# Kernel optimization log

Measured on AMD Instinct MI355X. Metric: run time of the kernel, lower is better.

## Reference

```python
import jax, jax.numpy as jnp
import numpy as np

B, T, D_IN, D_SAE, K = 256, 8, 768, 8192, 32


def setup_inputs() -> dict:
    key = jax.random.key(0)
    k1, k2, k3 = jax.random.split(key, 3)
    x = jax.random.normal(k1, (B, T, D_IN), dtype=jnp.float32)
    # kaiming_uniform: bound = sqrt(6 / fan_in), fan_in = prod of trailing dims
    bound_e = float(np.sqrt(6.0 / (D_SAE * D_IN)))
    W_enc = jax.random.uniform(k2, (T, D_SAE, D_IN), jnp.float32, -bound_e, bound_e)
    bound_d = float(np.sqrt(6.0 / (D_IN * D_SAE)))
    W_dec = jax.random.uniform(k3, (T, D_IN, D_SAE), jnp.float32, -bound_d, bound_d)
    # decoder column normalization (norm over d_in axis), as in _normalize_decoder
    norms = jnp.clip(jnp.linalg.norm(W_dec, axis=1, keepdims=True), 1e-8)
    W_dec = W_dec / norms
    b_enc = jnp.zeros((T, D_SAE), jnp.float32)
    b_dec = jnp.zeros((T, D_IN), jnp.float32)
    return {"x": x, "W_enc": W_enc, "b_enc": b_enc, "W_dec": W_dec,
            "b_dec": b_dec, "k": K}


def reference(x, W_enc, b_enc, W_dec, b_dec, k):
    # x: (B, T, d_in)
    x_c = x - b_dec[None]                                   # (B, T, d)
    pre = jnp.einsum('btd,thd->bth', x_c, W_enc) + b_enc[None]  # (B, T, h)
    bt = pre.shape[0] * pre.shape[1]
    pre_flat = pre.reshape(bt, -1)
    topk_vals, topk_idx = jax.lax.top_k(pre_flat, k)        # (BT, k)
    rows = jnp.arange(bt)[:, None]
    u_flat = jnp.zeros_like(pre_flat).at[rows, topk_idx].set(jax.nn.relu(topk_vals))
    u = u_flat.reshape(pre.shape)                            # (B, T, h)
    x_hat = jnp.einsum('bth,tdh->btd', u, W_dec) + b_dec[None]
    recon_loss = jnp.mean(jnp.sum((x_hat - x) ** 2, axis=-1))
    return recon_loss, x_hat, u
```

## Files before the change

### kernel.cpp

```cpp
#include <hip/hip_runtime.h>
#include <cstdint>
#include <cstddef>

constexpr int B_SZ  = 256;
constexpr int T_SZ  = 8;
constexpr int DIN   = 768;
constexpr int DSAE  = 8192;
constexpr int KSEL  = 32;
constexpr int NROWS = B_SZ * T_SZ;
constexpr int CAND_CAP = 64;
constexpr int RCAP  = 32;
constexpr float EPS_W = 2e-4f;

constexpr size_t XC_SZ    = (size_t)NROWS * DIN;
constexpr size_t OFF_XC   = 0;
constexpr size_t OFF_XCB  = OFF_XC + XC_SZ;
constexpr size_t XCB_WORDS = XC_SZ / 2;
constexpr size_t OFF_SIDX = OFF_XCB + XCB_WORDS;
constexpr size_t OFF_SVAL = OFF_SIDX + (size_t)NROWS * KSEL;
constexpr size_t OFF_WT   = OFF_SVAL + (size_t)NROWS * KSEL;
constexpr size_t WT_WORDS = (size_t)T_SZ * DSAE * DIN / 2;
constexpr size_t WS_FAST_WORDS = OFF_WT + WT_WORDS;

typedef short bf16x8 __attribute__((ext_vector_type(8)));
typedef float f32x4  __attribute__((ext_vector_type(4)));

__device__ inline unsigned rne1(float x) {
  unsigned u = __float_as_uint(x);
  return (u + 0x7FFFu + ((u >> 16) & 1u)) >> 16;
}
__device__ inline float bf16tof(unsigned short v) {
  return __uint_as_float((unsigned)v << 16);
}

__global__ void k_zero(float* p) { *p = 0.f; }

__global__ __launch_bounds__(256) void k_xc(const float* __restrict__ x,
                                            const float* __restrict__ bdec,
                                            float* __restrict__ xc,
                                            unsigned short* __restrict__ xcb) {
  int n = NROWS * DIN;
  for (int i = blockIdx.x * 256 + threadIdx.x; i < n; i += gridDim.x * 256) {
    int d = i % DIN;
    int t = (i / DIN) & (T_SZ - 1);
    float v = x[i] - bdec[t * DIN + d];
    xc[i] = v;
    xcb[i] = (unsigned short)rne1(v);
  }
}

__global__ __launch_bounds__(256, 4) void k_encoder(const unsigned short* __restrict__ xcb,
                                                    const float* __restrict__ Wenc,
                                                    const float* __restrict__ benc,
                                                    float* __restrict__ pre) {
  const int t  = blockIdx.y;
  const int n0 = blockIdx.x * 64;
  constexpr int NS = DIN / 32;
  __shared__ __align__(16) short Bs[2][64 * 32];
  const int tid = threadIdx.x;

  const int srow = tid >> 2;
  const int sq   = tid & 3;
  const float* bG = Wenc + ((size_t)t * DSAE + n0 + srow) * DIN + sq * 8;
  const int sssw = (srow & 3) ^ ((srow >> 2) & 3);
  const int wOff = srow * 32 + ((sq ^ sssw) << 3);
  float4 r0, r1;
  auto loadB = [&](int s) {
    const float* p = bG + s * 32;
    r0 = *(const float4*)p; r1 = *(const float4*)(p + 4);
  };
  auto stage = [&](int buf) {
    uint4 U;
    U.x = rne1(r0.x) | (rne1(r0.y) << 16); U.y = rne1(r0.z) | (rne1(r0.w) << 16);
    U.z = rne1(r1.x) | (rne1(r1.y) << 16); U.w = rne1(r1.z) | (rne1(r1.w) << 16);
    *(uint4*)&Bs[buf][wOff] = U;
  };

  const int wm = tid >> 6, lane = tid & 63;
  const int l15 = lane & 15, kc = lane >> 4;
  const unsigned short* aBase =
      xcb + ((size_t)(wm * 64 + l15) * T_SZ + t) * DIN + kc * 8;
  constexpr size_t A_MI = (size_t)16 * T_SZ * DIN;
  int bOff[4];
#pragma unroll
  for (int ni = 0; ni < 4; ++ni) {
    int row = ni * 16 + l15;
    bOff[ni] = row * 32 + ((kc ^ ((row & 3) ^ ((row >> 2) & 3))) << 3);
  }

  f32x4 acc[4][4] = {};
  bf16x8 a[4];
  loadB(0); stage(0); loadB(1);
#pragma unroll
  for (int mi = 0; mi < 4; ++mi)
    a[mi] = *(const bf16x8*)(aBase + mi * A_MI);
  int cur = 0;
  for (int s = 0; s < NS; ++s) {
    __syncthreads();
    bf16x8 bf[4];
#pragma unroll
    for (int ni = 0; ni < 4; ++ni) bf[ni] = *(const bf16x8*)&Bs[cur][bOff[ni]];
#pragma unroll
    for (int mi = 0; mi < 4; ++mi)
#pragma unroll
      for (int ni = 0; ni < 4; ++ni)
        acc[mi][ni] = __builtin_amdgcn_mfma_f32_16x16x32_bf16(
            a[mi], bf[ni], acc[mi][ni], 0, 0, 0);
    if (s + 1 < NS) {
      stage(cur ^ 1);
#pragma unroll
      for (int mi = 0; mi < 4; ++mi)
        a[mi] = *(const bf16x8*)(aBase + (s + 1) * 32 + mi * A_MI);
      if (s + 2 < NS) loadB(s + 2);
    }
    cur ^= 1;
  }

#pragma unroll
  for (int ni = 0; ni < 4; ++ni) {
    const int col = n0 + ni * 16 + l15;
    const float bias = benc[(size_t)t * DSAE + col];
#pragma unroll
    for (int mi = 0; mi < 4; ++mi) {
      const int rbase = wm * 64 + mi * 16 + kc * 4;
#pragma unroll
      for (int j = 0; j < 4; ++j)
        pre[((size_t)(rbase + j) * T_SZ + t) * DSAE + col] = acc[mi][ni][j] + bias;
    }
  }
}

__global__ __launch_bounds__(256) void k_select(const float* __restrict__ xc,
                                                const float* __restrict__ Wenc,
                                                const float* __restrict__ benc,
                                                float* u,
                                                int* __restrict__ sel_idx,
                                                float* __restrict__ sel_val) {
  const int r = blockIdx.x, t = r & (T_SZ - 1);
  __shared__ float sp[DSAE];
  __shared__ float redf[4], redf2[4];
  __shared__ int   redi[4];
  __shared__ float cv[CAND_CAP]; __shared__ int ci[CAND_CAP];
  __shared__ float sv[CAND_CAP]; __shared__ int si[CAND_CAP];
  __shared__ float rv[RCAP];     __shared__ int ri[RCAP];
  __shared__ double rd[RCAP];
  __shared__ double xd[DIN];
  __shared__ int   s_n, s_nR, s_A, s_nW;
  const int tid = threadIdx.x, lane = tid & 63, w = tid >> 6;
  float* urow = u + (size_t)r * DSAE;

  float s1 = 0.f, s2 = 0.f;
  for (int sgm = 0; sgm < DSAE / 256; ++sgm) {
    float v = urow[tid + sgm * 256];
    sp[tid + sgm * 256] = v;
    s1 += v; s2 = fmaf(v, v, s2);
  }
  for (int off = 32; off; off >>= 1) {
    s1 += __shfl_down(s1, off); s2 += __shfl_down(s2, off);
  }
  if (lane == 0) { redf[w] = s1; redf2[w] = s2; }
  __syncthreads();
  const float mean = (redf[0] + redf[1] + redf[2] + redf[3]) * (1.f / DSAE);
  const float var  = (redf2[0] + redf2[1] + redf2[2] + redf2[3]) * (1.f / DSAE) - mean * mean;
  const float sd   = sqrtf(fmaxf(var, 1e-20f));

  auto countGE = [&](float th) -> int {
    int c = 0;
#pragma unroll
    for (int sgm = 0; sgm < DSAE / 256; ++sgm)
      c += (sp[tid + sgm * 256] >= th) ? 1 : 0;
    for (int off = 32; off; off >>= 1) c += __shfl_down(c, off);
    __syncthreads();
    if (lane == 0) redi[w] = c;
    __syncthreads();
    return redi[0] + redi[1] + redi[2] + redi[3];
  };

  float tlo = mean + 2.0f * sd, thi = mean + 3.5f * sd;
  for (int it = 0; it < 8 && countGE(tlo) < KSEL; ++it) tlo -= sd;
  float th = mean + 2.52f * sd;
  int c = countGE(th);
  for (int it = 0; it < 24 && (c < KSEL || c > CAND_CAP); ++it) {
    if (c > CAND_CAP) tlo = th; else thi = th;
    th = 0.5f * (tlo + thi);
    c = countGE(th);
  }
  if (c < KSEL) { th = tlo; c = countGE(th); }

  if (tid == 0) s_n = 0;
  __syncthreads();
  for (int sgm = 0; sgm < DSAE / 256; ++sgm) {
    int i = tid + sgm * 256;
    float v = sp[i];
    if (v >= th) {
      int p = atomicAdd(&s_n, 1);
      if (p < CAND_CAP) { cv[p] = v; ci[p] = i; }
    }
  }
  __syncthreads();
  const int n = s_n < CAND_CAP ? s_n : CAND_CAP;

  if (tid < n) {
    float v = cv[tid]; int id = ci[tid];
    int rk = 0;
    for (int j = 0; j < n; ++j) {
      float vj = cv[j];
      rk += (vj > v || (vj == v && ci[j] < id)) ? 1 : 0;
    }
    sv[rk] = v; si[rk] = id;
  }
  __syncthreads();

  const float v32 = sv[KSEL - 1];
  const float wlo = v32 - EPS_W, whi = v32 + EPS_W;
  if (tid == 0) {
    int A = 0;
    while (A < KSEL - 1 && sv[A] > whi) ++A;
    s_A = A;
    int e = A;
    while (e < n && sv[e] >= wlo) ++e;
    s_nW = e - A;
  }
  __syncthreads();
  const int A  = s_A;
  const int nW = s_nW < RCAP ? s_nW : RCAP;
  if (tid < nW) { rv[tid] = sv[A + tid]; ri[tid] = si[A + tid]; }
  if (tid == 0) s_nR = nW;
  __syncthreads();
  if (th > wlo) {
    for (int sgm = 0; sgm < DSAE / 256; ++sgm) {
      int i = tid + sgm * 256;
      float v = sp[i];
      if (v >= wlo && v < th) {
        int p = atomicAdd(&s_nR, 1);
        if (p < RCAP) { rv[p] = v; ri[p] = i; }
      }
    }
  }
  __syncthreads();
  const int nR = s_nR < RCAP ? s_nR : RCAP;

  if (nR >= 2) {
    for (int i = tid; i < DIN; i += 256) xd[i] = (double)xc[(size_t)r * DIN + i];
    __syncthreads();
    for (int j = w; j < nR; j += 4) {
      const int h = ri[j];
      const float* wrow = Wenc + ((size_t)t * DSAE + h) * DIN;
      double s = 0.0;
#pragma unroll
      for (int ss = 0; ss < DIN / 64; ++ss)
        s += xd[lane + 64 * ss] * (double)wrow[lane + 64 * ss];
      for (int off = 32; off; off >>= 1) s += __shfl_down(s, off);
      if (lane == 0) rd[j] = s + (double)benc[(size_t)t * DSAE + h];
    }
  } else if (nR == 1) {
    if (tid == 0) rd[0] = (double)rv[0];
  }
  __syncthreads();

  for (int sgm = 0; sgm < DSAE / 256; ++sgm) urow[tid + sgm * 256] = 0.f;
  __syncthreads();

  if (tid < A) {
    float val = fmaxf(sv[tid], 0.f);
    urow[si[tid]] = val;
    sel_idx[(size_t)r * KSEL + tid] = si[tid];
    sel_val[(size_t)r * KSEL + tid] = val;
  }
  const int need = KSEL - A;
  if (tid < nR) {
    double v = rd[tid]; int id = ri[tid];
    int rk = 0;
    for (int j = 0; j < nR; ++j) {
      double vj = rd[j];
      rk += (vj > v || (vj == v && ri[j] < id)) ? 1 : 0;
    }
    if (rk < need) {
      float val = fmaxf((float)v, 0.f);
      urow[id] = val;
      sel_idx[(size_t)r * KSEL + A + rk] = id;
      sel_val[(size_t)r * KSEL + A + rk] = val;
    }
  }
}

__global__ __launch_bounds__(256) void k_transpose(const float* __restrict__ W,
                                                   unsigned short* __restrict__ Wt) {
  __shared__ float s[32][33];
  const int t  = blockIdx.z;
  const int h0 = blockIdx.x * 32;
  const int d0 = blockIdx.y * 32;
  const int c  = threadIdx.x & 31, rr = threadIdx.x >> 5;
#pragma unroll
  for (int q = 0; q < 4; ++q) {
    int d = d0 + rr + q * 8;
    s[rr + q * 8][c] = W[((size_t)t * DIN + d) * DSAE + h0 + c];
  }
  __syncthreads();
#pragma unroll
  for (int q = 0; q < 4; ++q) {
    int h = h0 + rr + q * 8;
    Wt[((size_t)t * DSAE + h) * DIN + d0 + c] = (unsigned short)rne1(s[c][rr + q * 8]);
  }
}

template <bool TRANSPOSED>
__global__ __launch_bounds__(256) void k_decoder(const void* __restrict__ Wd_,
                                                 const float* __restrict__ x,
                                                 const float* __restrict__ bdec,
                                                 const int* __restrict__ sel_idx,
                                                 const float* __restrict__ sel_val,
                                                 float* __restrict__ xhat,
                                                 float* __restrict__ loss) {
  const int r = blockIdx.x, t = r & (T_SZ - 1);
  __shared__ int   si[KSEL];
  __shared__ float sv[KSEL];
  __shared__ float rbuf[4];
  const int tid = threadIdx.x;
  if (tid < KSEL) {
    si[tid] = sel_idx[(size_t)r * KSEL + tid] & (DSAE - 1);
    sv[tid] = sel_val[(size_t)r * KSEL + tid];
  }
  __syncthreads();

  float acc[3];
#pragma unroll
  for (int i = 0; i < 3; ++i) acc[i] = bdec[(size_t)t * DIN + tid + 256 * i];
#pragma unroll 4
  for (int j = 0; j < KSEL; ++j) {
    const int h = si[j];
    const float v = sv[j];
    if (TRANSPOSED) {
      const unsigned short* wrow =
          (const unsigned short*)Wd_ + ((size_t)t * DSAE + h) * DIN;
#pragma unroll
      for (int i = 0; i < 3; ++i)
        acc[i] = fmaf(v, bf16tof(wrow[tid + 256 * i]), acc[i]);
    } else {
      const float* Wd = (const float*)Wd_;
#pragma unroll
      for (int i = 0; i < 3; ++i)
        acc[i] = fmaf(v, Wd[((size_t)t * DIN + tid + 256 * i) * DSAE + h], acc[i]);
    }
  }
  float sq = 0.f;
#pragma unroll
  for (int i = 0; i < 3; ++i) {
    const int d = tid + 256 * i;
    const float xv = x[(size_t)r * DIN + d];
    xhat[(size_t)r * DIN + d] = acc[i];
    const float e = acc[i] - xv;
    sq = fmaf(e, e, sq);
  }
  for (int off = 32; off; off >>= 1) sq += __shfl_down(sq, off);
  if ((tid & 63) == 0) rbuf[tid >> 6] = sq;
  __syncthreads();
  if (tid == 0)
    atomicAdd(loss, (rbuf[0] + rbuf[1] + rbuf[2] + rbuf[3]) * (1.0f / NROWS));
}

extern "C" void kernel_launch(void* const* d_in, const int* in_sizes, int n_in,
                              void* d_out, int out_size, void* d_ws, size_t ws_size,
                              hipStream_t stream) {
  const float* x    = (const float*)d_in[0];
  const float* Wenc = (const float*)d_in[1];
  const float* benc = (const float*)d_in[2];
  const float* Wdec = (const float*)d_in[3];
  const float* bdec = (const float*)d_in[4];

  float* out  = (float*)d_out;
  float* loss = out;
  float* xhat = out + 1;
  float* u    = out + 1 + (size_t)NROWS * DIN;

  float*          wsf  = (float*)d_ws;
  float*          xc   = wsf + OFF_XC;
  unsigned short* xcb  = (unsigned short*)(wsf + OFF_XCB);
  int*            sidx = (int*)(wsf + OFF_SIDX);
  float*          sval = wsf + OFF_SVAL;
  unsigned short* wt   = (unsigned short*)(wsf + OFF_WT);
  const bool fast = ws_size >= WS_FAST_WORDS * sizeof(float);

  k_zero<<<1, 1, 0, stream>>>(loss);
  k_xc<<<1536, 256, 0, stream>>>(x, bdec, xc, xcb);
  k_encoder<<<dim3(DSAE / 64, T_SZ), 256, 0, stream>>>(xcb, Wenc, benc, u);
  k_select<<<NROWS, 256, 0, stream>>>(xc, Wenc, benc, u, sidx, sval);
  if (fast) {
    k_transpose<<<dim3(DSAE / 32, DIN / 32, T_SZ), 256, 0, stream>>>(Wdec, wt);
    k_decoder<true><<<NROWS, 256, 0, stream>>>(wt, x, bdec, sidx, sval, xhat, loss);
  } else {
    k_decoder<false><<<NROWS, 256, 0, stream>>>(Wdec, x, bdec, sidx, sval, xhat, loss);
  }
}
```

Baseline: 258.7 us.

## Stream fp32 encoder weights directly into LDS and truncate to bf16 on read

The encoder GEMM now copies raw fp32 W_enc tiles straight from global memory into a swizzled LDS buffer with global_load_lds, skipping the register staging and round-to-nearest conversion. Weights are truncated to bf16 when read from LDS, and the A-operand loads move into the current iteration. The candidate tolerance EPS_W is widened to absorb the extra error from truncation. The goal is to cut VGPR pressure and conversion ALU in the prefetch path. The cost is double the LDS footprint and LDS read traffic, plus lower weight precision and a wider top-k candidate margin.

```diff
diff --git a/kernel.cpp b/kernel.cpp
--- a/kernel.cpp
+++ b/kernel.cpp
@@ -10,7 +10,7 @@
 constexpr int NROWS = B_SZ * T_SZ;
 constexpr int CAND_CAP = 64;
 constexpr int RCAP  = 32;
-constexpr float EPS_W = 2e-4f;
+constexpr float EPS_W = 3.2e-4f;
 
 constexpr size_t XC_SZ    = (size_t)NROWS * DIN;
 constexpr size_t OFF_XC   = 0;
@@ -31,6 +31,15 @@
 }
 __device__ inline float bf16tof(unsigned short v) {
   return __uint_as_float((unsigned)v << 16);
+}
+__device__ inline unsigned packtr(float a, float b) {
+  return (__float_as_uint(a) >> 16) | (__float_as_uint(b) & 0xFFFF0000u);
+}
+
+__device__ inline void gload_lds16(const void* g, void* l) {
+  __builtin_amdgcn_global_load_lds(
+      (const __attribute__((address_space(1))) void*)g,
+      (__attribute__((address_space(3))) void*)l, 16, 0, 0);
 }
 
 __global__ void k_zero(float* p) { *p = 0.f; }
@@ -56,24 +65,24 @@
   const int t  = blockIdx.y;
   const int n0 = blockIdx.x * 64;
   constexpr int NS = DIN / 32;
-  __shared__ __align__(16) short Bs[2][64 * 32];
+  __shared__ __align__(16) float Bs[2][64 * 32];
   const int tid = threadIdx.x;
 
-  const int srow = tid >> 2;
-  const int sq   = tid & 3;
-  const float* bG = Wenc + ((size_t)t * DSAE + n0 + srow) * DIN + sq * 8;
-  const int sssw = (srow & 3) ^ ((srow >> 2) & 3);
-  const int wOff = srow * 32 + ((sq ^ sssw) << 3);
-  float4 r0, r1;
-  auto loadB = [&](int s) {
-    const float* p = bG + s * 32;
-    r0 = *(const float4*)p; r1 = *(const float4*)(p + 4);
-  };
-  auto stage = [&](int buf) {
-    uint4 U;
-    U.x = rne1(r0.x) | (rne1(r0.y) << 16); U.y = rne1(r0.z) | (rne1(r0.w) << 16);
-    U.z = rne1(r1.x) | (rne1(r1.y) << 16); U.w = rne1(r1.z) | (rne1(r1.w) << 16);
-    *(uint4*)&Bs[buf][wOff] = U;
+  int gRow[2], gCol[2], ldsL[2];
+#pragma unroll
+  for (int i = 0; i < 2; ++i) {
+    int L = i * 4096 + tid * 16;
+    int G = L ^ (((L >> 7) & 7) << 4);
+    gRow[i] = G >> 7;
+    gCol[i] = (G & 127) >> 2;
+    ldsL[i] = L;
+  }
+  auto STAGE = [&](int buf, int s) {
+#pragma unroll
+    for (int i = 0; i < 2; ++i) {
+      const float* src = Wenc + ((size_t)t * DSAE + n0 + gRow[i]) * DIN + s * 32 + gCol[i];
+      gload_lds16(src, (char*)&Bs[buf][0] + ldsL[i]);
+    }
   };
 
   const int wm = tid >> 6, lane = tid & 63;
@@ -81,38 +90,43 @@
   const unsigned short* aBase =
       xcb + ((size_t)(wm * 64 + l15) * T_SZ + t) * DIN + kc * 8;
   constexpr size_t A_MI = (size_t)16 * T_SZ * DIN;
-  int bOff[4];
+  int bOff0[4], bOff1[4];
 #pragma unroll
   for (int ni = 0; ni < 4; ++ni) {
     int row = ni * 16 + l15;
-    bOff[ni] = row * 32 + ((kc ^ ((row & 3) ^ ((row >> 2) & 3))) << 3);
+    int P = row * 128 + kc * 32;
+    int sw = (row & 7) << 4;
+    bOff0[ni] = P ^ sw;
+    bOff1[ni] = (P + 16) ^ sw;
   }
 
   f32x4 acc[4][4] = {};
-  bf16x8 a[4];
-  loadB(0); stage(0); loadB(1);
-#pragma unroll
-  for (int mi = 0; mi < 4; ++mi)
-    a[mi] = *(const bf16x8*)(aBase + mi * A_MI);
+  STAGE(0, 0);
+  __syncthreads();
   int cur = 0;
   for (int s = 0; s < NS; ++s) {
-    __syncthreads();
+    if (s + 1 < NS) STAGE(cur ^ 1, s + 1);
+    bf16x8 a[4];
+#pragma unroll
+    for (int mi = 0; mi < 4; ++mi)
+      a[mi] = *(const bf16x8*)(aBase + s * 32 + mi * A_MI);
     bf16x8 bf[4];
 #pragma unroll
-    for (int ni = 0; ni < 4; ++ni) bf[ni] = *(const bf16x8*)&Bs[cur][bOff[ni]];
+    for (int ni = 0; ni < 4; ++ni) {
+      f32x4 f0 = *(const f32x4*)((const char*)&Bs[cur][0] + bOff0[ni]);
+      f32x4 f1 = *(const f32x4*)((const char*)&Bs[cur][0] + bOff1[ni]);
+      union { uint32_t u[4]; bf16x8 h; } cv;
+      cv.u[0] = packtr(f0.x, f0.y); cv.u[1] = packtr(f0.z, f0.w);
+      cv.u[2] = packtr(f1.x, f1.y); cv.u[3] = packtr(f1.z, f1.w);
+      bf[ni] = cv.h;
+    }
 #pragma unroll
     for (int mi = 0; mi < 4; ++mi)
 #pragma unroll
       for (int ni = 0; ni < 4; ++ni)
         acc[mi][ni] = __builtin_amdgcn_mfma_f32_16x16x32_bf16(
             a[mi], bf[ni], acc[mi][ni], 0, 0, 0);
-    if (s + 1 < NS) {
-      stage(cur ^ 1);
-#pragma unroll
-      for (int mi = 0; mi < 4; ++mi)
-        a[mi] = *(const bf16x8*)(aBase + (s + 1) * 32 + mi * A_MI);
-      if (s + 2 < NS) loadB(s + 2);
-    }
+    __syncthreads();
     cur ^= 1;
   }
 
```

New measurement: 259.1 us. No clear change (+0.2%).
